# Kernel tuning notes

Hardware: AMD Instinct MI355X
Metric: run time of the kernel (lower is better)

Reference implementation:

```python
import jax, jax.numpy as jnp
import numpy as np

B, S, D, H = 2, 2048, 1024, 16
MASK_VAL = -50000.0

def setup_inputs() -> dict:
    key = jax.random.key(0)
    k1, k2, k3, k4 = jax.random.split(key, 4)
    # weights stored as [in, out] so projection is x @ W (equals torch Linear with W.T)
    s = 1.0 / np.sqrt(D)
    return {
        "x": jax.random.normal(k1, (B, S, D), dtype=jnp.float32),
        "Wq": jax.random.normal(k2, (D, D), dtype=jnp.float32) * s,
        "Wkv": jax.random.normal(k3, (D, 2 * D), dtype=jnp.float32) * s,
        "Wo": jax.random.normal(k4, (D, D), dtype=jnp.float32) * s,
    }

def reference(x, Wq, Wkv, Wo):
    b, sl, d = x.shape
    h = H
    hd = d // h
    scale = hd ** (-0.5)
    q = x @ Wq                      # [b, sl, d]
    kv = x @ Wkv                    # [b, sl, 2d]
    k, v = jnp.split(kv, 2, axis=-1)
    # [b, h, s, hd]
    q = q.reshape(b, sl, h, hd).transpose(0, 2, 1, 3)
    k = k.reshape(b, sl, h, hd).transpose(0, 2, 1, 3)
    v = v.reshape(b, sl, h, hd).transpose(0, 2, 1, 3)
    dots = jnp.einsum('bhid,bhjd->bhij', q * scale, k)  # [b,h,s,s]
    # causal: strictly-upper-triangular entries set to MASK_VAL
    causal = jnp.tril(jnp.ones((sl, sl), dtype=bool))
    dots = jnp.where(causal, dots, MASK_VAL)
    attn = jax.nn.softmax(dots, axis=-1)
    out = jnp.einsum('bhij,bhjd->bihd', attn, v).reshape(b, sl, d)
    return out @ Wo
```

## Files before the change

### kernel.cpp

```cpp
#include <hip/hip_runtime.h>

typedef __bf16 bf16_t;
typedef unsigned short u16;
typedef __attribute__((ext_vector_type(8))) __bf16 bf16x8;
typedef __attribute__((ext_vector_type(4))) float f32x4;
typedef __attribute__((ext_vector_type(4))) u16 u16x4;
typedef __attribute__((ext_vector_type(8))) u16 u16x8;

#define SS 2048
#define PSTR 72

__device__ __forceinline__ u16 f2b(float f) {
    return __builtin_bit_cast(u16, (__bf16)f);
}

__device__ __forceinline__ float fexp2(float x) {
#if __has_builtin(__builtin_amdgcn_exp2f)
    return __builtin_amdgcn_exp2f(x);
#else
    float r;
    asm("v_exp_f32 %0, %1" : "=v"(r) : "v"(x));
    return r;
#endif
}

__device__ __forceinline__ void async_copy16(const u16* g, u16* l) {
    __builtin_amdgcn_global_load_lds(
        (__attribute__((address_space(1))) void*)(u16*)g,
        (__attribute__((address_space(3))) void*)l, 16, 0, 0);
}

__device__ __forceinline__ bf16x8 ldfrag(const u16* p) {
    return __builtin_bit_cast(bf16x8, *(const u16x8*)p);
}

__global__ __launch_bounds__(256)
void cast_x_kernel(const float* __restrict__ x, u16* __restrict__ xb) {
    size_t i = ((size_t)blockIdx.x * 256 + threadIdx.x) * 8;
    float4 a = *(const float4*)(x + i);
    float4 b = *(const float4*)(x + i + 4);
    u16x8 o;
    o[0] = f2b(a.x); o[1] = f2b(a.y); o[2] = f2b(a.z); o[3] = f2b(a.w);
    o[4] = f2b(b.x); o[5] = f2b(b.y); o[6] = f2b(b.z); o[7] = f2b(b.w);
    *(u16x8*)(xb + i) = o;
}

__global__ __launch_bounds__(256)
void transpose_all(const float* __restrict__ Wq, const float* __restrict__ Wkv,
                   const float* __restrict__ Wo, u16* __restrict__ WcatT,
                   u16* __restrict__ WoT) {
    const int z = blockIdx.z;
    if (z != 1 && blockIdx.y >= 16) return;
    const float* src; u16* dst; int N; float scale;
    if (z == 0)      { src = Wq;  dst = WcatT;               N = 1024; scale = 0.125f * 1.44269504089f; }
    else if (z == 1) { src = Wkv; dst = WcatT + 1024 * 1024; N = 2048; scale = 1.0f; }
    else             { src = Wo;  dst = WoT;                 N = 1024; scale = 1.0f; }
    __shared__ __attribute__((aligned(16))) u16 tile[64][72];
    const int k0 = blockIdx.x * 64, n0 = blockIdx.y * 64;
    const int tid = threadIdx.x;
#pragma unroll
    for (int p = 0; p < 4; ++p) {
        int c = p * 256 + tid;
        int r = c >> 4, c4 = c & 15;
        float4 v = *(const float4*)(src + (size_t)(k0 + r) * N + n0 + c4 * 4);
        u16x4 o;
        o[0] = f2b(v.x * scale); o[1] = f2b(v.y * scale);
        o[2] = f2b(v.z * scale); o[3] = f2b(v.w * scale);
        *(u16x4*)&tile[r][c4 * 4] = o;
    }
    __syncthreads();
#pragma unroll
    for (int p = 0; p < 4; ++p) {
        int c = p * 256 + tid;
        int n = c >> 4, k4 = c & 15;
        u16x4 o;
#pragma unroll
        for (int i = 0; i < 4; ++i) o[i] = tile[k4 * 4 + i][n];
        *(u16x4*)(dst + (size_t)(n0 + n) * 1024 + k0 + k4 * 4) = o;
    }
}

__global__ __launch_bounds__(256)
void transpose_v(const u16* __restrict__ QKV, u16* __restrict__ VTg) {
    __shared__ __attribute__((aligned(16))) u16 tile[64][72];
    const int s0 = blockIdx.x * 64;
    const int bh = blockIdx.y;
    const int b = bh >> 4, h = bh & 15;
    const int tid = threadIdx.x;
    const u16* src = QKV + ((size_t)b * SS + s0) * 3072 + 2048 + h * 64;
#pragma unroll
    for (int p = 0; p < 4; ++p) {
        int c = p * 256 + tid;
        int s = c >> 4, h4 = c & 15;
        *(u16x4*)&tile[s][h4 * 4] = *(const u16x4*)(src + (size_t)s * 3072 + h4 * 4);
    }
    __syncthreads();
    u16* dst = VTg + (size_t)bh * 64 * 2048 + s0;
#pragma unroll
    for (int p = 0; p < 4; ++p) {
        int c = p * 256 + tid;
        int hd = c >> 4, s4 = c & 15;
        u16x4 o;
#pragma unroll
        for (int i = 0; i < 4; ++i) o[i] = tile[s4 * 4 + i][hd];
        *(u16x4*)(dst + (size_t)hd * 2048 + s4 * 4) = o;
    }
}

template <typename OutT>
__global__ __launch_bounds__(256, 2)
void gemm_bt(const u16* __restrict__ A, const u16* __restrict__ BT,
             OutT* __restrict__ C, int M, int N, int K) {
    __shared__ __attribute__((aligned(16))) u16 As[128 * 32];
    __shared__ __attribute__((aligned(16))) u16 Bs[128 * 32];
    const int tid = threadIdx.x;
    const int wave = tid >> 6, lane = tid & 63;
    const int l15 = lane & 15, quad = lane >> 4;
    const int m0 = blockIdx.y * 128, n0 = blockIdx.x * 128;
    const int wm = (wave >> 1) * 64, wn = (wave & 1) * 64;
    const f32x4 zero = {0.f, 0.f, 0.f, 0.f};
    f32x4 acc[4][4];
#pragma unroll
    for (int i = 0; i < 4; ++i)
#pragma unroll
        for (int j = 0; j < 4; ++j) acc[i][j] = zero;
    const int r0 = tid >> 2, kc = (tid & 3) * 8;
    for (int k0 = 0; k0 < K; k0 += 32) {
        async_copy16(A + (size_t)(m0 + r0) * K + k0 + kc, As + tid * 8);
        async_copy16(BT + (size_t)(n0 + r0) * K + k0 + kc, Bs + tid * 8);
        async_copy16(A + (size_t)(m0 + 64 + r0) * K + k0 + kc, As + (256 + tid) * 8);
        async_copy16(BT + (size_t)(n0 + 64 + r0) * K + k0 + kc, Bs + (256 + tid) * 8);
        __syncthreads();
        bf16x8 af[4], bf[4];
#pragma unroll
        for (int t = 0; t < 4; ++t) {
            af[t] = ldfrag(As + (wm + t * 16 + l15) * 32 + quad * 8);
            bf[t] = ldfrag(Bs + (wn + t * 16 + l15) * 32 + quad * 8);
        }
#pragma unroll
        for (int mt = 0; mt < 4; ++mt)
#pragma unroll
            for (int nt = 0; nt < 4; ++nt)
                acc[mt][nt] = __builtin_amdgcn_mfma_f32_16x16x32_bf16(
                    af[mt], bf[nt], acc[mt][nt], 0, 0, 0);
        __syncthreads();
    }
#pragma unroll
    for (int mt = 0; mt < 4; ++mt)
#pragma unroll
        for (int nt = 0; nt < 4; ++nt) {
            const int n = n0 + wn + nt * 16 + l15;
#pragma unroll
            for (int r = 0; r < 4; ++r) {
                const int m = m0 + wm + mt * 16 + quad * 4 + r;
                float v = acc[mt][nt][r];
                if constexpr (sizeof(OutT) == 2) C[(size_t)m * N + n] = (OutT)f2b(v);
                else                             C[(size_t)m * N + n] = v;
            }
        }
}

__global__ __launch_bounds__(256, 2)
void gemm_bt64(const u16* __restrict__ A, const u16* __restrict__ BT,
               float* __restrict__ C, int M, int N, int K) {
    __shared__ __attribute__((aligned(16))) u16 As[128 * 32];
    __shared__ __attribute__((aligned(16))) u16 Bs[64 * 32];
    const int tid = threadIdx.x;
    const int wave = tid >> 6, lane = tid & 63;
    const int l15 = lane & 15, quad = lane >> 4;
    const int m0 = blockIdx.y * 128, n0 = blockIdx.x * 64;
    const int wm = (wave >> 1) * 64, wn = (wave & 1) * 32;
    const f32x4 zero = {0.f, 0.f, 0.f, 0.f};
    f32x4 acc[4][2];
#pragma unroll
    for (int i = 0; i < 4; ++i)
#pragma unroll
        for (int j = 0; j < 2; ++j) acc[i][j] = zero;
    const int r0 = tid >> 2, kc = (tid & 3) * 8;
    for (int k0 = 0; k0 < K; k0 += 32) {
        async_copy16(A + (size_t)(m0 + r0) * K + k0 + kc, As + tid * 8);
        async_copy16(A + (size_t)(m0 + 64 + r0) * K + k0 + kc, As + (256 + tid) * 8);
        async_copy16(BT + (size_t)(n0 + r0) * K + k0 + kc, Bs + tid * 8);
        __syncthreads();
        bf16x8 af[4], bf[2];
#pragma unroll
        for (int t = 0; t < 4; ++t)
            af[t] = ldfrag(As + (wm + t * 16 + l15) * 32 + quad * 8);
#pragma unroll
        for (int t = 0; t < 2; ++t)
            bf[t] = ldfrag(Bs + (wn + t * 16 + l15) * 32 + quad * 8);
#pragma unroll
        for (int mt = 0; mt < 4; ++mt)
#pragma unroll
            for (int nt = 0; nt < 2; ++nt)
                acc[mt][nt] = __builtin_amdgcn_mfma_f32_16x16x32_bf16(
                    af[mt], bf[nt], acc[mt][nt], 0, 0, 0);
        __syncthreads();
    }
#pragma unroll
    for (int mt = 0; mt < 4; ++mt)
#pragma unroll
        for (int nt = 0; nt < 2; ++nt) {
            const int n = n0 + wn + nt * 16 + l15;
#pragma unroll
            for (int r = 0; r < 4; ++r) {
                const int m = m0 + wm + mt * 16 + quad * 4 + r;
                C[(size_t)m * N + n] = acc[mt][nt][r];
            }
        }
}

__device__ __forceinline__ void attn_score_softmax(
    const bf16x8 (&qf)[2], const bf16x8 (&kf)[4][2],
    float (&l_i)[4], u16* __restrict__ P, int wq, int kv0, int l15, int quad) {
    const f32x4 cinit = {-10.f, -10.f, -10.f, -10.f};
    f32x4 S[4];
#pragma unroll
    for (int nt = 0; nt < 4; ++nt) {
        f32x4 a = __builtin_amdgcn_mfma_f32_16x16x32_bf16(qf[0], kf[nt][0], cinit, 0, 0, 0);
        S[nt] = __builtin_amdgcn_mfma_f32_16x16x32_bf16(qf[1], kf[nt][1], a, 0, 0, 0);
    }
    if (kv0 + 63 > wq) {
#pragma unroll
        for (int nt = 0; nt < 4; ++nt)
#pragma unroll
            for (int r = 0; r < 4; ++r) {
                int qa = wq + quad * 4 + r;
                int ka = kv0 + nt * 16 + l15;
                if (ka > qa) S[nt][r] = -1e30f;
            }
    }
#pragma unroll
    for (int nt = 0; nt < 4; ++nt)
#pragma unroll
        for (int r = 0; r < 4; ++r) {
            float pv = fexp2(S[nt][r]);
            l_i[r] += pv;
            P[(quad * 4 + r) * PSTR + nt * 16 + l15] = f2b(pv);
        }
}

__device__ __forceinline__ void attn_pv(
    const u16* __restrict__ P, const bf16x8 (&vf)[4][2],
    f32x4 (&O)[4], int l15, int quad) {
    bf16x8 pf0 = ldfrag(P + l15 * PSTR + quad * 8);
    bf16x8 pf1 = ldfrag(P + l15 * PSTR + 32 + quad * 8);
#pragma unroll
    for (int nt = 0; nt < 4; ++nt) {
        O[nt] = __builtin_amdgcn_mfma_f32_16x16x32_bf16(pf0, vf[nt][0], O[nt], 0, 0, 0);
        O[nt] = __builtin_amdgcn_mfma_f32_16x16x32_bf16(pf1, vf[nt][1], O[nt], 0, 0, 0);
    }
}

__global__ __launch_bounds__(256, 2)
void attn_kernel(const u16* __restrict__ QKV, const u16* __restrict__ VTg,
                 u16* __restrict__ AO) {
    __shared__ __attribute__((aligned(16))) u16 Kt[2][2 * 64 * 32];
    __shared__ __attribute__((aligned(16))) u16 Vt[2][2 * 64 * 32];
    __shared__ __attribute__((aligned(16))) u16 Pq[128 * PSTR];
    const int tid = threadIdx.x;
    const int wave = tid >> 6, lane = tid & 63;
    const int l15 = lane & 15, quad = lane >> 4;
    const int bh = blockIdx.y, b = bh >> 4, h = bh & 15;
    const int xe = b ? 15 - (int)blockIdx.x : (int)blockIdx.x;
    const int qbA = 31 - xe, qbB = xe;
    const int qA0 = qbA * 64, qB0 = qbB * 64;
    const size_t bS = (size_t)b * SS;
    const u16* vbase = VTg + (size_t)bh * 64 * 2048;
    const int rr = (tid >> 2) & 63, kc8 = (tid & 3) * 8;

    {
        const u16* qsrcA = QKV + (bS + qA0 + rr) * 3072 + h * 64 + kc8;
        async_copy16(qsrcA,      Pq + tid * 8);
        async_copy16(qsrcA + 32, Pq + (256 + tid) * 8);
        const u16* qsrcB = QKV + (bS + qB0 + rr) * 3072 + h * 64 + kc8;
        async_copy16(qsrcB,      Pq + (512 + tid) * 8);
        async_copy16(qsrcB + 32, Pq + (768 + tid) * 8);
        const u16* ksrc = QKV + (bS + rr) * 3072 + 1024 + h * 64 + kc8;
        async_copy16(ksrc,      Kt[0] + tid * 8);
        async_copy16(ksrc + 32, Kt[0] + (256 + tid) * 8);
        const u16* vsrc = vbase + (size_t)rr * 2048 + kc8;
        async_copy16(vsrc,      Vt[0] + tid * 8);
        async_copy16(vsrc + 32, Vt[0] + (256 + tid) * 8);
    }
    __syncthreads();
    bf16x8 qfA[2], qfB[2];
#pragma unroll
    for (int ks = 0; ks < 2; ++ks) {
        qfA[ks] = ldfrag(Pq + ks * 2048 + (wave * 16 + l15) * 32 + quad * 8);
        qfB[ks] = ldfrag(Pq + 4096 + ks * 2048 + (wave * 16 + l15) * 32 + quad * 8);
    }
    __syncthreads();

    const int wqA = qA0 + wave * 16, wqB = qB0 + wave * 16;
    u16* PA = Pq + (wave * 16) * PSTR;
    u16* PB = Pq + (64 + wave * 16) * PSTR;
    float lA[4], lB[4];
    f32x4 OA[4], OB[4];
    const f32x4 zero = {0.f, 0.f, 0.f, 0.f};
#pragma unroll
    for (int r = 0; r < 4; ++r) { lA[r] = lB[r] = 0.f; }
#pragma unroll
    for (int nt = 0; nt < 4; ++nt) { OA[nt] = zero; OB[nt] = zero; }

    for (int j = 0; j <= qbA; ++j) {
        if (j < qbA) {
            const int kv1 = (j + 1) * 64;
            const int nb = (j + 1) & 1;
            const u16* ksrc = QKV + (bS + kv1 + rr) * 3072 + 1024 + h * 64 + kc8;
            async_copy16(ksrc,      Kt[nb] + tid * 8);
            async_copy16(ksrc + 32, Kt[nb] + (256 + tid) * 8);
            const u16* vsrc = vbase + (size_t)rr * 2048 + kv1 + kc8;
            async_copy16(vsrc,      Vt[nb] + tid * 8);
            async_copy16(vsrc + 32, Vt[nb] + (256 + tid) * 8);
        }
        const int kv0 = j * 64;
        const bool bAct = (j <= qbB);
        const u16* KB = Kt[j & 1];
        const u16* VB = Vt[j & 1];
        bf16x8 kf[4][2];
#pragma unroll
        for (int nt = 0; nt < 4; ++nt)
#pragma unroll
            for (int ks = 0; ks < 2; ++ks)
                kf[nt][ks] = ldfrag(KB + ks * 2048 + (nt * 16 + l15) * 32 + quad * 8);
        attn_score_softmax(qfA, kf, lA, PA, wqA, kv0, l15, quad);
        if (bAct)
            attn_score_softmax(qfB, kf, lB, PB, wqB, kv0, l15, quad);
        bf16x8 vf[4][2];
#pragma unroll
        for (int nt = 0; nt < 4; ++nt)
#pragma unroll
            for (int ks = 0; ks < 2; ++ks)
                vf[nt][ks] = ldfrag(VB + ks * 2048 + (nt * 16 + l15) * 32 + quad * 8);
        attn_pv(PA, vf, OA, l15, quad);
        if (bAct)
            attn_pv(PB, vf, OB, l15, quad);
        __syncthreads();
    }
#pragma unroll
    for (int r = 0; r < 4; ++r) {
        float sA = lA[r];
        sA += __shfl_xor(sA, 1); sA += __shfl_xor(sA, 2);
        sA += __shfl_xor(sA, 4); sA += __shfl_xor(sA, 8);
        float sB = lB[r];
        sB += __shfl_xor(sB, 1); sB += __shfl_xor(sB, 2);
        sB += __shfl_xor(sB, 4); sB += __shfl_xor(sB, 8);
        float invA = 1.0f / sA;
        float invB = 1.0f / sB;
        size_t rowA = bS + (size_t)wqA + quad * 4 + r;
        size_t rowB = bS + (size_t)wqB + quad * 4 + r;
#pragma unroll
        for (int nt = 0; nt < 4; ++nt) {
            AO[rowA * 1024 + h * 64 + nt * 16 + l15] = f2b(OA[nt][r] * invA);
            AO[rowB * 1024 + h * 64 + nt * 16 + l15] = f2b(OB[nt][r] * invB);
        }
    }
}

extern "C" void kernel_launch(void* const* d_in, const int* in_sizes, int n_in,
                              void* d_out, int out_size, void* d_ws, size_t ws_size,
                              hipStream_t stream) {
    (void)in_sizes; (void)n_in; (void)out_size; (void)ws_size;
    const float* x   = (const float*)d_in[0];
    const float* Wq  = (const float*)d_in[1];
    const float* Wkv = (const float*)d_in[2];
    const float* Wo  = (const float*)d_in[3];
    float* out = (float*)d_out;
    char* ws = (char*)d_ws;
    u16* xb    = (u16*)(ws);
    u16* WcatT = (u16*)(ws + (size_t)(8 << 20));
    u16* WoT   = (u16*)(ws + (size_t)(14 << 20));
    u16* QKV   = (u16*)(ws + (size_t)(16 << 20));
    u16* VTb   = (u16*)(ws + (size_t)(40 << 20));
    u16* AO    = xb;

    cast_x_kernel<<<2048, 256, 0, stream>>>(x, xb);
    transpose_all<<<dim3(16, 32, 3), 256, 0, stream>>>(Wq, Wkv, Wo, WcatT, WoT);
    gemm_bt<u16><<<dim3(24, 32), 256, 0, stream>>>(xb, WcatT, QKV, 4096, 3072, 1024);
    transpose_v<<<dim3(32, 32), 256, 0, stream>>>(QKV, VTb);
    attn_kernel<<<dim3(16, 32), 256, 0, stream>>>(QKV, VTb, AO);
    gemm_bt64<<<dim3(16, 32), 256, 0, stream>>>(AO, WoT, out, 4096, 1024, 1024);
}
```

Before: 185.2 us.

## Compute transposed score tiles per wave over key slices to cut K fragment loads

```diff
diff --git a/kernel.cpp b/kernel.cpp
--- a/kernel.cpp
+++ b/kernel.cpp
@@ -210,34 +210,30 @@
         }
 }
 
-__device__ __forceinline__ void attn_score_softmax(
-    const bf16x8 (&qf)[2], const bf16x8 (&kf)[4][2],
-    float (&l_i)[4], u16* __restrict__ P, int wq, int kv0, int l15, int quad) {
+__device__ __forceinline__ void attn_scoreT(
+    const bf16x8 (&kf)[2], const bf16x8 (&qf)[4][2],
+    float (&l_i)[4], u16* __restrict__ P, bool diag, int w16, int l15, int quad) {
     const f32x4 cinit = {-10.f, -10.f, -10.f, -10.f};
-    f32x4 S[4];
-#pragma unroll
-    for (int nt = 0; nt < 4; ++nt) {
-        f32x4 a = __builtin_amdgcn_mfma_f32_16x16x32_bf16(qf[0], kf[nt][0], cinit, 0, 0, 0);
-        S[nt] = __builtin_amdgcn_mfma_f32_16x16x32_bf16(qf[1], kf[nt][1], a, 0, 0, 0);
-    }
-    if (kv0 + 63 > wq) {
-#pragma unroll
-        for (int nt = 0; nt < 4; ++nt)
-#pragma unroll
-            for (int r = 0; r < 4; ++r) {
-                int qa = wq + quad * 4 + r;
-                int ka = kv0 + nt * 16 + l15;
-                if (ka > qa) S[nt][r] = -1e30f;
-            }
-    }
-#pragma unroll
-    for (int nt = 0; nt < 4; ++nt)
+#pragma unroll
+    for (int t = 0; t < 4; ++t) {
+        f32x4 a = __builtin_amdgcn_mfma_f32_16x16x32_bf16(kf[0], qf[t][0], cinit, 0, 0, 0);
+        f32x4 s = __builtin_amdgcn_mfma_f32_16x16x32_bf16(kf[1], qf[t][1], a, 0, 0, 0);
+        if (diag) {
+#pragma unroll
+            for (int r = 0; r < 4; ++r)
+                if (w16 + quad * 4 + r > t * 16 + l15) s[r] = -1e30f;
+        }
+        u16x4 pk;
+        float acc = 0.f;
 #pragma unroll
         for (int r = 0; r < 4; ++r) {
-            float pv = fexp2(S[nt][r]);
-            l_i[r] += pv;
-            P[(quad * 4 + r) * PSTR + nt * 16 + l15] = f2b(pv);
-        }
+            float pv = fexp2(s[r]);
+            acc += pv;
+            pk[r] = f2b(pv);
+        }
+        l_i[t] += acc;
+        *(u16x4*)(P + (t * 16 + l15) * PSTR + w16 + quad * 4) = pk;
+    }
 }
 
 __device__ __forceinline__ void attn_pv(
@@ -261,6 +257,7 @@
     const int tid = threadIdx.x;
     const int wave = tid >> 6, lane = tid & 63;
     const int l15 = lane & 15, quad = lane >> 4;
+    const int w16 = wave * 16;
     const int bh = blockIdx.y, b = bh >> 4, h = bh & 15;
     const int xe = b ? 15 - (int)blockIdx.x : (int)blockIdx.x;
     const int qbA = 31 - xe, qbB = xe;
@@ -284,22 +281,23 @@
         async_copy16(vsrc + 32, Vt[0] + (256 + tid) * 8);
     }
     __syncthreads();
-    bf16x8 qfA[2], qfB[2];
-#pragma unroll
-    for (int ks = 0; ks < 2; ++ks) {
-        qfA[ks] = ldfrag(Pq + ks * 2048 + (wave * 16 + l15) * 32 + quad * 8);
-        qfB[ks] = ldfrag(Pq + 4096 + ks * 2048 + (wave * 16 + l15) * 32 + quad * 8);
-    }
-    __syncthreads();
-
-    const int wqA = qA0 + wave * 16, wqB = qB0 + wave * 16;
-    u16* PA = Pq + (wave * 16) * PSTR;
-    u16* PB = Pq + (64 + wave * 16) * PSTR;
+    bf16x8 qfA[4][2], qfB[4][2];
+#pragma unroll
+    for (int t = 0; t < 4; ++t)
+#pragma unroll
+        for (int ks = 0; ks < 2; ++ks) {
+            qfA[t][ks] = ldfrag(Pq + ks * 2048 + (t * 16 + l15) * 32 + quad * 8);
+            qfB[t][ks] = ldfrag(Pq + 4096 + ks * 2048 + (t * 16 + l15) * 32 + quad * 8);
+        }
+    __syncthreads();
+
+    u16* PA = Pq;
+    u16* PB = Pq + 64 * PSTR;
     float lA[4], lB[4];
     f32x4 OA[4], OB[4];
     const f32x4 zero = {0.f, 0.f, 0.f, 0.f};
 #pragma unroll
-    for (int r = 0; r < 4; ++r) { lA[r] = lB[r] = 0.f; }
+    for (int t = 0; t < 4; ++t) { lA[t] = lB[t] = 0.f; }
 #pragma unroll
     for (int nt = 0; nt < 4; ++nt) { OA[nt] = zero; OB[nt] = zero; }
 
@@ -314,42 +312,51 @@
             async_copy16(vsrc,      Vt[nb] + tid * 8);
             async_copy16(vsrc + 32, Vt[nb] + (256 + tid) * 8);
         }
-        const int kv0 = j * 64;
         const bool bAct = (j <= qbB);
         const u16* KB = Kt[j & 1];
         const u16* VB = Vt[j & 1];
-        bf16x8 kf[4][2];
-#pragma unroll
-        for (int nt = 0; nt < 4; ++nt)
-#pragma unroll
-            for (int ks = 0; ks < 2; ++ks)
-                kf[nt][ks] = ldfrag(KB + ks * 2048 + (nt * 16 + l15) * 32 + quad * 8);
-        attn_score_softmax(qfA, kf, lA, PA, wqA, kv0, l15, quad);
+        bf16x8 kf[2];
+#pragma unroll
+        for (int ks = 0; ks < 2; ++ks)
+            kf[ks] = ldfrag(KB + ks * 2048 + (w16 + l15) * 32 + quad * 8);
+        attn_scoreT(kf, qfA, lA, PA, j == qbA, w16, l15, quad);
         if (bAct)
-            attn_score_softmax(qfB, kf, lB, PB, wqB, kv0, l15, quad);
+            attn_scoreT(kf, qfB, lB, PB, j == qbB, w16, l15, quad);
+        __syncthreads();
         bf16x8 vf[4][2];
 #pragma unroll
         for (int nt = 0; nt < 4; ++nt)
 #pragma unroll
             for (int ks = 0; ks < 2; ++ks)
                 vf[nt][ks] = ldfrag(VB + ks * 2048 + (nt * 16 + l15) * 32 + quad * 8);
-        attn_pv(PA, vf, OA, l15, quad);
+        attn_pv(PA + w16 * PSTR, vf, OA, l15, quad);
         if (bAct)
-            attn_pv(PB, vf, OB, l15, quad);
-        __syncthreads();
-    }
+            attn_pv(PB + w16 * PSTR, vf, OB, l15, quad);
+        __syncthreads();
+    }
+
+    float* lsh = (float*)Kt;
+#pragma unroll
+    for (int t = 0; t < 4; ++t) {
+        float sA = lA[t];
+        sA += __shfl_xor(sA, 16); sA += __shfl_xor(sA, 32);
+        float sB = lB[t];
+        sB += __shfl_xor(sB, 16); sB += __shfl_xor(sB, 32);
+        if (lane < 16) {
+            lsh[(t * 16 + l15) * 4 + wave] = sA;
+            lsh[(64 + t * 16 + l15) * 4 + wave] = sB;
+        }
+    }
+    __syncthreads();
 #pragma unroll
     for (int r = 0; r < 4; ++r) {
-        float sA = lA[r];
-        sA += __shfl_xor(sA, 1); sA += __shfl_xor(sA, 2);
-        sA += __shfl_xor(sA, 4); sA += __shfl_xor(sA, 8);
-        float sB = lB[r];
-        sB += __shfl_xor(sB, 1); sB += __shfl_xor(sB, 2);
-        sB += __shfl_xor(sB, 4); sB += __shfl_xor(sB, 8);
-        float invA = 1.0f / sA;
-        float invB = 1.0f / sB;
-        size_t rowA = bS + (size_t)wqA + quad * 4 + r;
-        size_t rowB = bS + (size_t)wqB + quad * 4 + r;
+        const int qlA = w16 + quad * 4 + r;
+        f32x4 la = *(const f32x4*)&lsh[qlA * 4];
+        f32x4 lb = *(const f32x4*)&lsh[(64 + qlA) * 4];
+        float invA = 1.0f / (la[0] + la[1] + la[2] + la[3]);
+        float invB = 1.0f / (lb[0] + lb[1] + lb[2] + lb[3]);
+        size_t rowA = bS + (size_t)qA0 + qlA;
+        size_t rowB = bS + (size_t)qB0 + qlA;
 #pragma unroll
         for (int nt = 0; nt < 4; ++nt) {
             AO[rowA * 1024 + h * 64 + nt * 16 + l15] = f2b(OA[nt][r] * invA);
```

Measured after the change: 183.5 us. No clear change (-1.0%).
